# Kernel optimization log

Hardware: AMD Instinct MI355X
Metric: run time of the kernel (lower is better)

Reference implementation:

```python
import jax, jax.numpy as jnp
import numpy as np

K = 30               # max_iter
RHO = 1e-12
POWER_ITERS = 5
MU_INSIDE = 1e-3
ALPHA_FEAS_TOL = 1e-7
EPS_INSIDE = 1e-6


def setup_inputs() -> dict:
    key = jax.random.key(0)
    k1, k2, k3 = jax.random.split(key, 3)
    B, S, m, n = 16, 32, 256, 256
    A = jax.random.normal(k1, (B, S, m, n), dtype=jnp.float32)
    # shift b positive-ish so some constraints are feasible / some violated
    b = jax.random.normal(k2, (B, S, m), dtype=jnp.float32) + 1.0
    x = jax.random.normal(k3, (B, S, n), dtype=jnp.float32)
    return {"x": x, "A": A, "b": b}


def _project(x, A, b):
    # Row-normalize constraints: A_w[b,s,i,:] has unit norm
    row_norm = jnp.maximum(jnp.linalg.norm(A, axis=-1, keepdims=True), 1e-12)
    A_w = A / row_norm                       # [B,S,m,n]
    b_w = b / row_norm[..., 0]               # [B,S,m]
    b_tight = b_w - MU_INSIDE

    # Deterministic spectral eta via power iteration on A^T A
    Bn, Sn, m, n = A.shape
    v = jnp.ones((Bn, Sn, n, 1), dtype=A.dtype)
    v = v / (jnp.linalg.norm(v, axis=-2, keepdims=True) + 1e-12)
    At = jnp.swapaxes(A_w, -2, -1)
    for _ in range(POWER_ITERS):
        Av = A_w @ v
        AtAv = At @ Av
        v = AtAv / (jnp.linalg.norm(AtAv, axis=-2, keepdims=True) + 1e-12)
    Av = A_w @ v
    eta = (1.0 / (jnp.sum(Av * Av, axis=(-2, -1)) + RHO))[..., None]  # [B,S,1]

    # Stage 1: K-step UVP on tightened constraints
    def step(x_, _):
        r = jnp.einsum('bsmn,bsn->bsm', A_w, x_) - b_tight
        g = jnp.einsum('bsmn,bsm->bsn', A_w, jax.nn.relu(r))
        return x_ - eta * g, None
    x_uvp, _ = jax.lax.scan(step, x, None, length=K)

    # Stage 2: alpha-map from UVP anchor toward original x, gated by feasibility
    Ax = jnp.einsum('bsmn,bsn->bsm', A_w, x_uvp)
    max_viol = jnp.max(jnp.maximum(Ax - b_w, 0.0), axis=-1, keepdims=True)
    do_alpha = max_viol <= ALPHA_FEAS_TOL

    d = x - x_uvp
    Ad = jnp.einsum('bsmn,bsn->bsm', A_w, d)
    slack = b_w - Ax
    alpha_i = jnp.where(Ad > 0, slack / (Ad + 1e-12), jnp.inf)
    alpha = jnp.min(alpha_i, axis=-1, keepdims=True)
    alpha = jnp.where(jnp.isfinite(alpha), alpha, 1.0)
    alpha = jnp.clip(alpha - EPS_INSIDE, 0.0, 1.0)
    x_alpha = x_uvp + alpha * d
    return jnp.where(do_alpha, x_alpha, x_uvp)


def reference(x, A, b):
    return _project(x, A, b)
```

## Files before the change

kernel.cpp:

```cpp
#include <hip/hip_runtime.h>
#include <math.h>

#define N 256
#define PSTR 257


__global__ __launch_bounds__(1024) void icvp_kernel(
    const float* __restrict__ X, const float* __restrict__ A,
    const float* __restrict__ Bv, float* __restrict__ out)
{
  const int p  = blockIdx.x;
  const int t  = threadIdx.x;
  const int ti = t >> 5;
  const int tj = t & 31;
  const bool rdr = (t < 256);
  const int rk = t & 31;
  const int rc = (t >> 5) & 7;
  const int ridx = rk * 8 + rc;
  const int w  = t >> 6;

  __shared__ __align__(16) float part[8224];
  __shared__ __align__(16) float xn[256];
  __shared__ __align__(16) float x0n[256];
  __shared__ __align__(16) float dn[256];
  __shared__ __align__(16) float rn[256];
  __shared__ __align__(16) float invn[256];
  __shared__ float btp[256];
  __shared__ float bwp[256];
  __shared__ float scal[12];

  float Areg[8][8];
  {
    const float* Ap = A + (size_t)p * (N * N);
    #pragma unroll
    for (int r = 0; r < 8; ++r) {
      const float4* src = reinterpret_cast<const float4*>(Ap + (ti * 8 + r) * N + tj * 8);
      float4 a0 = src[0];
      float4 a1 = src[1];
      Areg[r][0] = a0.x; Areg[r][1] = a0.y; Areg[r][2] = a0.z; Areg[r][3] = a0.w;
      Areg[r][4] = a1.x; Areg[r][5] = a1.y; Areg[r][6] = a1.z; Areg[r][7] = a1.w;
    }
  }
  float b_raw = 0.f;
  if (rdr) {
    float xv = X[p * N + t];
    xn[t]  = xv;
    x0n[t] = xv;
    b_raw  = Bv[p * N + ridx];
  }

  auto fwd_store = [&](const float (&vl)[8]) {
    #pragma unroll
    for (int r = 0; r < 8; ++r) {
      float s = 0.f;
      #pragma unroll
      for (int c = 0; c < 8; ++c) s = fmaf(Areg[r][c], vl[c], s);
      part[tj * PSTR + r * 32 + ti] = s;
    }
  };
  auto trans_store = [&](const float (&rl)[8]) {
    #pragma unroll
    for (int c = 0; c < 8; ++c) {
      float s = 0.f;
      #pragma unroll
      for (int r = 0; r < 8; ++r) s = fmaf(Areg[r][c], rl[r], s);
      part[ti * PSTR + c * 32 + tj] = s;
    }
  };
  auto red32 = [&]() {
    float s0 = 0.f, s1 = 0.f, s2 = 0.f, s3 = 0.f;
    const int off = rc * 32 + rk;
    #pragma unroll
    for (int q = 0; q < 8; ++q) {
      s0 += part[(4 * q + 0) * PSTR + off];
      s1 += part[(4 * q + 1) * PSTR + off];
      s2 += part[(4 * q + 2) * PSTR + off];
      s3 += part[(4 * q + 3) * PSTR + off];
    }
    return (s0 + s1) + (s2 + s3);
  };
  auto load8 = [&](const float* base, float (&dst)[8], int idx8) {
    const float4* v4 = reinterpret_cast<const float4*>(base + idx8 * 8);
    float4 a0 = v4[0], a1 = v4[1];
    dst[0] = a0.x; dst[1] = a0.y; dst[2] = a0.z; dst[3] = a0.w;
    dst[4] = a1.x; dst[5] = a1.y; dst[6] = a1.z; dst[7] = a1.w;
  };

  #pragma unroll
  for (int r = 0; r < 8; ++r) {
    float s = 0.f;
    #pragma unroll
    for (int c = 0; c < 8; ++c) s = fmaf(Areg[r][c], Areg[r][c], s);
    part[tj * PSTR + r * 32 + ti] = s;
  }
  __syncthreads();
  if (rdr) {
    float s = red32();
    float nrm = fmaxf(sqrtf(s), 1e-12f);
    float inv = 1.0f / nrm;
    invn[ridx] = inv;
    float bw = b_raw * inv;
    bwp[rc * 32 + rk] = bw;
    btp[rc * 32 + rk] = bw - 1e-3f;
  }
  __syncthreads();
  {
    float invl[8];
    load8(invn, invl, ti);
    #pragma unroll
    for (int r = 0; r < 8; ++r)
      #pragma unroll
      for (int c = 0; c < 8; ++c) Areg[r][c] *= invl[r];
  }

  float vloc[8];
  #pragma unroll
  for (int c = 0; c < 8; ++c) vloc[c] = 0.0625f;

  for (int pit = 0; pit < 5; ++pit) {
    fwd_store(vloc);
    __syncthreads();
    if (rdr) rn[ridx] = red32();
    __syncthreads();
    float rl[8];
    load8(rn, rl, ti);
    trans_store(rl);
    __syncthreads();
    if (rdr) {
      float g = red32();
      dn[ridx] = g;
      float ss = g * g;
      #pragma unroll
      for (int m = 1; m < 64; m <<= 1) ss += __shfl_xor(ss, m);
      if ((t & 63) == 0) scal[4 + w] = ss;
    }
    __syncthreads();
    if (t == 0) {
      float s = scal[4] + scal[5] + scal[6] + scal[7];
      scal[0] = sqrtf(s) + 1e-12f;
    }
    __syncthreads();
    {
      float dl[8];
      load8(dn, dl, tj);
      float den = scal[0];
      #pragma unroll
      for (int c = 0; c < 8; ++c) vloc[c] = dl[c] / den;
    }
  }
  fwd_store(vloc);
  __syncthreads();
  if (rdr) {
    float av = red32();
    float ss = av * av;
    #pragma unroll
    for (int m = 1; m < 64; m <<= 1) ss += __shfl_xor(ss, m);
    if ((t & 63) == 0) scal[4 + w] = ss;
  }
  __syncthreads();
  if (t == 0) scal[1] = 1.0f / (scal[4] + scal[5] + scal[6] + scal[7] + 1e-12f);
  __syncthreads();
  const float eta = scal[1];

  float xloc[8];
  load8(xn, xloc, tj);
  for (int k = 0; k < 30; ++k) {
    fwd_store(xloc);
    __syncthreads();
    if (rdr) {
      float y = red32();
      rn[ridx] = fmaxf(y - btp[rc * 32 + rk], 0.f);
    }
    __syncthreads();
    float rl[8];
    load8(rn, rl, ti);
    trans_store(rl);
    __syncthreads();
    if (rdr) {
      float g = red32();
      xn[ridx] -= eta * g;
    }
    __syncthreads();
    load8(xn, xloc, tj);
  }

  fwd_store(xloc);
  __syncthreads();
  float slack = 0.f;
  if (rdr) {
    float ax = red32();
    float bw = bwp[rc * 32 + rk];
    slack = bw - ax;
    float mv = fmaxf(ax - bw, 0.f);
    #pragma unroll
    for (int m = 1; m < 64; m <<= 1) mv = fmaxf(mv, __shfl_xor(mv, m));
    if ((t & 63) == 0) scal[4 + w] = mv;
    dn[ridx] = x0n[ridx] - xn[ridx];
  }
  __syncthreads();
  if (t == 0) scal[2] = fmaxf(fmaxf(scal[4], scal[5]), fmaxf(scal[6], scal[7]));
  __syncthreads();
  float dloc[8];
  load8(dn, dloc, tj);
  fwd_store(dloc);
  __syncthreads();
  if (rdr) {
    float ad = red32();
    float ai = (ad > 0.f) ? slack / (ad + 1e-12f) : INFINITY;
    #pragma unroll
    for (int m = 1; m < 64; m <<= 1) ai = fminf(ai, __shfl_xor(ai, m));
    if ((t & 63) == 0) scal[8 + w] = ai;
  }
  __syncthreads();
  if (t == 0) {
    float al = fminf(fminf(scal[8], scal[9]), fminf(scal[10], scal[11]));
    if (!isfinite(al)) al = 1.0f;
    al = fminf(fmaxf(al - 1e-6f, 0.f), 1.0f);
    scal[3] = al;
  }
  __syncthreads();
  if (rdr) {
    float alpha = scal[3];
    bool da = (scal[2] <= 1e-7f);
    float xv = xn[t];
    out[p * N + t] = da ? fmaf(alpha, dn[t], xv) : xv;
  }
}

extern "C" void kernel_launch(void* const* d_in, const int* in_sizes, int n_in,
                              void* d_out, int out_size, void* d_ws, size_t ws_size,
                              hipStream_t stream) {
  const float* X  = (const float*)d_in[0];
  const float* A  = (const float*)d_in[1];
  const float* Bv = (const float*)d_in[2];
  float* out = (float*)d_out;
  const int nprob = in_sizes[0] / N;
  icvp_kernel<<<nprob, 1024, 0, stream>>>(X, A, Bv, out);
}
```

Before: 303.2 us.

## Replace shared-memory partial-sum reductions with in-wave swizzle reductions

```diff
diff --git a/kernel.cpp b/kernel.cpp
--- a/kernel.cpp
+++ b/kernel.cpp
@@ -2,32 +2,49 @@
 #include <math.h>
 
 #define N 256
-#define PSTR 257
-
-
-__global__ __launch_bounds__(1024) void icvp_kernel(
+#define PSTR 260
+
+template<int XM>
+__device__ __forceinline__ float swz(float v) {
+  int i = __builtin_amdgcn_ds_swizzle(__builtin_bit_cast(int, v), (XM << 10) | 0x1F);
+  return __builtin_bit_cast(float, i);
+}
+__device__ __forceinline__ float half_sum(float v) {
+  v += swz<1>(v); v += swz<2>(v); v += swz<4>(v); v += swz<8>(v); v += swz<16>(v);
+  return v;
+}
+__device__ __forceinline__ float wave_sum(float v) {
+  v = half_sum(v); v += __shfl_xor(v, 32); return v;
+}
+__device__ __forceinline__ float wave_max(float v) {
+  v = fmaxf(v, swz<1>(v)); v = fmaxf(v, swz<2>(v)); v = fmaxf(v, swz<4>(v));
+  v = fmaxf(v, swz<8>(v)); v = fmaxf(v, swz<16>(v)); v = fmaxf(v, __shfl_xor(v, 32));
+  return v;
+}
+__device__ __forceinline__ float wave_min(float v) {
+  v = fminf(v, swz<1>(v)); v = fminf(v, swz<2>(v)); v = fminf(v, swz<4>(v));
+  v = fminf(v, swz<8>(v)); v = fminf(v, swz<16>(v)); v = fminf(v, __shfl_xor(v, 32));
+  return v;
+}
+
+__global__ __launch_bounds__(1024, 4) void icvp_kernel(
     const float* __restrict__ X, const float* __restrict__ A,
     const float* __restrict__ Bv, float* __restrict__ out)
 {
-  const int p  = blockIdx.x;
-  const int t  = threadIdx.x;
-  const int ti = t >> 5;
-  const int tj = t & 31;
-  const bool rdr = (t < 256);
-  const int rk = t & 31;
-  const int rc = (t >> 5) & 7;
-  const int ridx = rk * 8 + rc;
-  const int w  = t >> 6;
-
-  __shared__ __align__(16) float part[8224];
-  __shared__ __align__(16) float xn[256];
-  __shared__ __align__(16) float x0n[256];
-  __shared__ __align__(16) float dn[256];
-  __shared__ __align__(16) float rn[256];
-  __shared__ __align__(16) float invn[256];
-  __shared__ float btp[256];
-  __shared__ float bwp[256];
-  __shared__ float scal[12];
+  const int p    = blockIdx.x;
+  const int t    = threadIdx.x;
+  const int ti   = t >> 5;
+  const int tj   = t & 31;
+  const int w    = t >> 6;
+  const int lane = t & 63;
+  const int q    = t & 3;
+  const int colr = t >> 2;
+
+  __shared__ __align__(16) float part[16 * PSTR];
+  __shared__ __align__(16) float xn[N];
+  __shared__ __align__(16) float x0n[N];
+  __shared__ __align__(16) float gn[N];
+  __shared__ float wsc[16], wsc2[16], scal[4];
 
   float Areg[8][8];
   {
@@ -35,82 +52,29 @@
     #pragma unroll
     for (int r = 0; r < 8; ++r) {
       const float4* src = reinterpret_cast<const float4*>(Ap + (ti * 8 + r) * N + tj * 8);
-      float4 a0 = src[0];
-      float4 a1 = src[1];
+      float4 a0 = src[0], a1 = src[1];
       Areg[r][0] = a0.x; Areg[r][1] = a0.y; Areg[r][2] = a0.z; Areg[r][3] = a0.w;
       Areg[r][4] = a1.x; Areg[r][5] = a1.y; Areg[r][6] = a1.z; Areg[r][7] = a1.w;
     }
   }
-  float b_raw = 0.f;
-  if (rdr) {
-    float xv = X[p * N + t];
-    xn[t]  = xv;
-    x0n[t] = xv;
-    b_raw  = Bv[p * N + ridx];
-  }
-
-  auto fwd_store = [&](const float (&vl)[8]) {
-    #pragma unroll
-    for (int r = 0; r < 8; ++r) {
-      float s = 0.f;
-      #pragma unroll
-      for (int c = 0; c < 8; ++c) s = fmaf(Areg[r][c], vl[c], s);
-      part[tj * PSTR + r * 32 + ti] = s;
-    }
-  };
-  auto trans_store = [&](const float (&rl)[8]) {
-    #pragma unroll
-    for (int c = 0; c < 8; ++c) {
-      float s = 0.f;
-      #pragma unroll
-      for (int r = 0; r < 8; ++r) s = fmaf(Areg[r][c], rl[r], s);
-      part[ti * PSTR + c * 32 + tj] = s;
-    }
-  };
-  auto red32 = [&]() {
-    float s0 = 0.f, s1 = 0.f, s2 = 0.f, s3 = 0.f;
-    const int off = rc * 32 + rk;
-    #pragma unroll
-    for (int q = 0; q < 8; ++q) {
-      s0 += part[(4 * q + 0) * PSTR + off];
-      s1 += part[(4 * q + 1) * PSTR + off];
-      s2 += part[(4 * q + 2) * PSTR + off];
-      s3 += part[(4 * q + 3) * PSTR + off];
-    }
-    return (s0 + s1) + (s2 + s3);
-  };
-  auto load8 = [&](const float* base, float (&dst)[8], int idx8) {
-    const float4* v4 = reinterpret_cast<const float4*>(base + idx8 * 8);
-    float4 a0 = v4[0], a1 = v4[1];
-    dst[0] = a0.x; dst[1] = a0.y; dst[2] = a0.z; dst[3] = a0.w;
-    dst[4] = a1.x; dst[5] = a1.y; dst[6] = a1.z; dst[7] = a1.w;
-  };
-
-  #pragma unroll
-  for (int r = 0; r < 8; ++r) {
-    float s = 0.f;
-    #pragma unroll
-    for (int c = 0; c < 8; ++c) s = fmaf(Areg[r][c], Areg[r][c], s);
-    part[tj * PSTR + r * 32 + ti] = s;
-  }
-  __syncthreads();
-  if (rdr) {
-    float s = red32();
-    float nrm = fmaxf(sqrtf(s), 1e-12f);
-    float inv = 1.0f / nrm;
-    invn[ridx] = inv;
-    float bw = b_raw * inv;
-    bwp[rc * 32 + rk] = bw;
-    btp[rc * 32 + rk] = bw - 1e-3f;
-  }
-  __syncthreads();
-  {
-    float invl[8];
-    load8(invn, invl, ti);
-    #pragma unroll
-    for (int r = 0; r < 8; ++r)
-      #pragma unroll
-      for (int c = 0; c < 8; ++c) Areg[r][c] *= invl[r];
+  if (t < N) { float xv = X[p * N + t]; xn[t] = xv; x0n[t] = xv; }
+
+  float btl[8];
+  {
+    const float4* bp = reinterpret_cast<const float4*>(Bv + p * N + ti * 8);
+    float4 b0 = bp[0], b1 = bp[1];
+    float bl[8] = {b0.x, b0.y, b0.z, b0.w, b1.x, b1.y, b1.z, b1.w};
+    #pragma unroll
+    for (int r = 0; r < 8; ++r) {
+      float s = 0.f;
+      #pragma unroll
+      for (int c = 0; c < 8; ++c) s = fmaf(Areg[r][c], Areg[r][c], s);
+      s = half_sum(s);
+      float inv = 1.0f / fmaxf(sqrtf(s), 1e-12f);
+      #pragma unroll
+      for (int c = 0; c < 8; ++c) Areg[r][c] *= inv;
+      btl[r] = bl[r] * inv - 1e-3f;
+    }
   }
 
   float vloc[8];
@@ -118,112 +82,164 @@
   for (int c = 0; c < 8; ++c) vloc[c] = 0.0625f;
 
   for (int pit = 0; pit < 5; ++pit) {
-    fwd_store(vloc);
-    __syncthreads();
-    if (rdr) rn[ridx] = red32();
-    __syncthreads();
+    float av[8];
+    #pragma unroll
+    for (int r = 0; r < 8; ++r) {
+      float s = 0.f;
+      #pragma unroll
+      for (int c = 0; c < 8; ++c) s = fmaf(Areg[r][c], vloc[c], s);
+      av[r] = half_sum(s);
+    }
+    float gc[8];
+    #pragma unroll
+    for (int c = 0; c < 8; ++c) {
+      float s = 0.f;
+      #pragma unroll
+      for (int r = 0; r < 8; ++r) s = fmaf(Areg[r][c], av[r], s);
+      s += __shfl_xor(s, 32);
+      gc[c] = s;
+    }
+    if (lane < 32) {
+      float4* dst = reinterpret_cast<float4*>(&part[w * PSTR + tj * 8]);
+      dst[0] = make_float4(gc[0], gc[1], gc[2], gc[3]);
+      dst[1] = make_float4(gc[4], gc[5], gc[6], gc[7]);
+    }
+    __syncthreads();
+    float g = (part[(q * 4 + 0) * PSTR + colr] + part[(q * 4 + 1) * PSTR + colr])
+            + (part[(q * 4 + 2) * PSTR + colr] + part[(q * 4 + 3) * PSTR + colr]);
+    g += __shfl_xor(g, 1); g += __shfl_xor(g, 2);
+    float ss = (q == 0) ? g * g : 0.f;
+    ss = wave_sum(ss);
+    if (lane == 0) wsc[w] = ss;
+    if (q == 0) gn[colr] = g;
+    __syncthreads();
+    if (t == 0) {
+      float s = 0.f;
+      #pragma unroll
+      for (int i = 0; i < 16; ++i) s += wsc[i];
+      scal[0] = sqrtf(s) + 1e-12f;
+    }
+    __syncthreads();
+    {
+      const float4* gp = reinterpret_cast<const float4*>(&gn[tj * 8]);
+      float4 g0 = gp[0], g1 = gp[1];
+      float den = scal[0];
+      vloc[0] = g0.x / den; vloc[1] = g0.y / den; vloc[2] = g0.z / den; vloc[3] = g0.w / den;
+      vloc[4] = g1.x / den; vloc[5] = g1.y / den; vloc[6] = g1.z / den; vloc[7] = g1.w / den;
+    }
+  }
+  {
+    float ss = 0.f;
+    #pragma unroll
+    for (int r = 0; r < 8; ++r) {
+      float s = 0.f;
+      #pragma unroll
+      for (int c = 0; c < 8; ++c) s = fmaf(Areg[r][c], vloc[c], s);
+      s = half_sum(s);
+      ss = fmaf(s, s, ss);
+    }
+    ss = wave_sum(ss);
+    if (lane == 0) wsc[w] = ss;
+    __syncthreads();
+    if (t == 0) {
+      float s = 0.f;
+      #pragma unroll
+      for (int i = 0; i < 16; ++i) s += wsc[i];
+      scal[1] = 1.0f / (s * 0.03125f + 1e-12f);
+    }
+    __syncthreads();
+  }
+  const float eta = scal[1];
+
+  float xloc[8];
+  {
+    const float4* xp = reinterpret_cast<const float4*>(&xn[tj * 8]);
+    float4 x0 = xp[0], x1 = xp[1];
+    xloc[0] = x0.x; xloc[1] = x0.y; xloc[2] = x0.z; xloc[3] = x0.w;
+    xloc[4] = x1.x; xloc[5] = x1.y; xloc[6] = x1.z; xloc[7] = x1.w;
+  }
+  for (int k = 0; k < 30; ++k) {
     float rl[8];
-    load8(rn, rl, ti);
-    trans_store(rl);
-    __syncthreads();
-    if (rdr) {
-      float g = red32();
-      dn[ridx] = g;
-      float ss = g * g;
-      #pragma unroll
-      for (int m = 1; m < 64; m <<= 1) ss += __shfl_xor(ss, m);
-      if ((t & 63) == 0) scal[4 + w] = ss;
-    }
-    __syncthreads();
-    if (t == 0) {
-      float s = scal[4] + scal[5] + scal[6] + scal[7];
-      scal[0] = sqrtf(s) + 1e-12f;
-    }
+    #pragma unroll
+    for (int r = 0; r < 8; ++r) {
+      float s = 0.f;
+      #pragma unroll
+      for (int c = 0; c < 8; ++c) s = fmaf(Areg[r][c], xloc[c], s);
+      s = half_sum(s);
+      rl[r] = fmaxf(s - btl[r], 0.f);
+    }
+    float gc[8];
+    #pragma unroll
+    for (int c = 0; c < 8; ++c) {
+      float s = 0.f;
+      #pragma unroll
+      for (int r = 0; r < 8; ++r) s = fmaf(Areg[r][c], rl[r], s);
+      s += __shfl_xor(s, 32);
+      gc[c] = s;
+    }
+    if (lane < 32) {
+      float4* dst = reinterpret_cast<float4*>(&part[w * PSTR + tj * 8]);
+      dst[0] = make_float4(gc[0], gc[1], gc[2], gc[3]);
+      dst[1] = make_float4(gc[4], gc[5], gc[6], gc[7]);
+    }
+    __syncthreads();
+    float g = (part[(q * 4 + 0) * PSTR + colr] + part[(q * 4 + 1) * PSTR + colr])
+            + (part[(q * 4 + 2) * PSTR + colr] + part[(q * 4 + 3) * PSTR + colr]);
+    g += __shfl_xor(g, 1); g += __shfl_xor(g, 2);
+    if (q == 0) xn[colr] = xn[colr] - eta * g;
     __syncthreads();
     {
-      float dl[8];
-      load8(dn, dl, tj);
-      float den = scal[0];
-      #pragma unroll
-      for (int c = 0; c < 8; ++c) vloc[c] = dl[c] / den;
-    }
-  }
-  fwd_store(vloc);
-  __syncthreads();
-  if (rdr) {
-    float av = red32();
-    float ss = av * av;
-    #pragma unroll
-    for (int m = 1; m < 64; m <<= 1) ss += __shfl_xor(ss, m);
-    if ((t & 63) == 0) scal[4 + w] = ss;
-  }
-  __syncthreads();
-  if (t == 0) scal[1] = 1.0f / (scal[4] + scal[5] + scal[6] + scal[7] + 1e-12f);
-  __syncthreads();
-  const float eta = scal[1];
-
-  float xloc[8];
-  load8(xn, xloc, tj);
-  for (int k = 0; k < 30; ++k) {
-    fwd_store(xloc);
-    __syncthreads();
-    if (rdr) {
-      float y = red32();
-      rn[ridx] = fmaxf(y - btp[rc * 32 + rk], 0.f);
-    }
-    __syncthreads();
-    float rl[8];
-    load8(rn, rl, ti);
-    trans_store(rl);
-    __syncthreads();
-    if (rdr) {
-      float g = red32();
-      xn[ridx] -= eta * g;
-    }
-    __syncthreads();
-    load8(xn, xloc, tj);
-  }
-
-  fwd_store(xloc);
-  __syncthreads();
-  float slack = 0.f;
-  if (rdr) {
-    float ax = red32();
-    float bw = bwp[rc * 32 + rk];
-    slack = bw - ax;
-    float mv = fmaxf(ax - bw, 0.f);
-    #pragma unroll
-    for (int m = 1; m < 64; m <<= 1) mv = fmaxf(mv, __shfl_xor(mv, m));
-    if ((t & 63) == 0) scal[4 + w] = mv;
-    dn[ridx] = x0n[ridx] - xn[ridx];
-  }
-  __syncthreads();
-  if (t == 0) scal[2] = fmaxf(fmaxf(scal[4], scal[5]), fmaxf(scal[6], scal[7]));
-  __syncthreads();
+      const float4* xp = reinterpret_cast<const float4*>(&xn[tj * 8]);
+      float4 x0 = xp[0], x1 = xp[1];
+      xloc[0] = x0.x; xloc[1] = x0.y; xloc[2] = x0.z; xloc[3] = x0.w;
+      xloc[4] = x1.x; xloc[5] = x1.y; xloc[6] = x1.z; xloc[7] = x1.w;
+    }
+  }
+
   float dloc[8];
-  load8(dn, dloc, tj);
-  fwd_store(dloc);
-  __syncthreads();
-  if (rdr) {
-    float ad = red32();
-    float ai = (ad > 0.f) ? slack / (ad + 1e-12f) : INFINITY;
-    #pragma unroll
-    for (int m = 1; m < 64; m <<= 1) ai = fminf(ai, __shfl_xor(ai, m));
-    if ((t & 63) == 0) scal[8 + w] = ai;
-  }
+  {
+    const float4* xp = reinterpret_cast<const float4*>(&x0n[tj * 8]);
+    float4 x0 = xp[0], x1 = xp[1];
+    dloc[0] = x0.x - xloc[0]; dloc[1] = x0.y - xloc[1];
+    dloc[2] = x0.z - xloc[2]; dloc[3] = x0.w - xloc[3];
+    dloc[4] = x1.x - xloc[4]; dloc[5] = x1.y - xloc[5];
+    dloc[6] = x1.z - xloc[6]; dloc[7] = x1.w - xloc[7];
+  }
+  float mv = 0.f, aim = INFINITY;
+  #pragma unroll
+  for (int r = 0; r < 8; ++r) {
+    float sx = 0.f, sd = 0.f;
+    #pragma unroll
+    for (int c = 0; c < 8; ++c) {
+      sx = fmaf(Areg[r][c], xloc[c], sx);
+      sd = fmaf(Areg[r][c], dloc[c], sd);
+    }
+    float ax = half_sum(sx);
+    float ad = half_sum(sd);
+    float bw = btl[r] + 1e-3f;
+    mv = fmaxf(mv, ax - bw);
+    float ai = (ad > 0.f) ? (bw - ax) / (ad + 1e-12f) : INFINITY;
+    aim = fminf(aim, ai);
+  }
+  mv = fmaxf(mv, 0.f);
+  mv  = wave_max(mv);
+  aim = wave_min(aim);
+  if (lane == 0) { wsc[w] = mv; wsc2[w] = aim; }
   __syncthreads();
   if (t == 0) {
-    float al = fminf(fminf(scal[8], scal[9]), fminf(scal[10], scal[11]));
-    if (!isfinite(al)) al = 1.0f;
-    al = fminf(fmaxf(al - 1e-6f, 0.f), 1.0f);
-    scal[3] = al;
+    float M = 0.f, Al = INFINITY;
+    #pragma unroll
+    for (int i = 0; i < 16; ++i) { M = fmaxf(M, wsc[i]); Al = fminf(Al, wsc2[i]); }
+    if (!isfinite(Al)) Al = 1.0f;
+    Al = fminf(fmaxf(Al - 1e-6f, 0.f), 1.0f);
+    scal[2] = M; scal[3] = Al;
   }
   __syncthreads();
-  if (rdr) {
-    float alpha = scal[3];
-    bool da = (scal[2] <= 1e-7f);
+  if (t < N) {
     float xv = xn[t];
-    out[p * N + t] = da ? fmaf(alpha, dn[t], xv) : xv;
+    float d  = x0n[t] - xv;
+    bool da  = (scal[2] <= 1e-7f);
+    out[p * N + t] = da ? fmaf(scal[3], d, xv) : xv;
   }
 }
 
```

Measured after the change: 335.4 us. +10.6%, slower.
